# Kernel optimization log

Hardware: AMD Instinct MI355X
Metric: run time of the kernel (lower is better)

Reference implementation:

```python
import jax, jax.numpy as jnp
from jax import lax
import numpy as np

B, N, C = 64, 8732, 81  # batch, anchors (SSD300), classes (COCO+bg)
POS_RATE = 0.003        # keep 3*num_pos < N (argsort column index must be in range)


def setup_inputs() -> dict:
    key = jax.random.key(0)
    k1, k2, k3, k4, k5, k6 = jax.random.split(key, 6)
    pred_conf = jax.random.normal(k1, (B, N, C), dtype=jnp.float32)
    pred_loc = jax.random.normal(k2, (B, N, 4), dtype=jnp.float32)
    # one-hot gt_conf; class 0 = background; sparse positives
    is_pos = jax.random.uniform(k3, (B, N)) < POS_RATE
    labels = jnp.where(is_pos, jax.random.randint(k4, (B, N), 1, C), 0)
    gt_conf = jax.nn.one_hot(labels, C, dtype=jnp.float32)
    gt_loc = jax.random.normal(k5, (B, N, 4), dtype=jnp.float32)
    return {"pred_conf": pred_conf, "pred_loc": pred_loc,
            "gt_conf": gt_conf, "gt_loc": gt_loc}


def reference(pred_conf, pred_loc, gt_conf, gt_loc):
    negative_ratio = 3.0
    # softmax cross entropy per anchor: [B, N]
    log_sm = jax.nn.log_softmax(pred_conf, axis=-1)
    conf_loss = -jnp.sum(log_sm * gt_conf, axis=-1)

    # positive mask (gt background prob == 0 => positive); detached in original
    pos_mask = (lax.stop_gradient(gt_conf)[:, :, 0] == 0).astype(jnp.float32)
    num_pos = jnp.sum(pos_mask)
    positive_conf_loss = pos_mask * conf_loss

    # hard-negative mining (faithful to original, including the quirk that the
    # "threshold" is the argsort INDEX value at column num_negative_conf)
    neg_mask = 1.0 - pos_mask
    cl_neg = lax.stop_gradient(conf_loss) * neg_mask  # detached in original
    order = jnp.argsort(cl_neg, axis=-1)              # [B, N] ascending
    num_neg = (negative_ratio * num_pos).astype(jnp.int32)  # scalar, traced
    idx = jnp.broadcast_to(num_neg, (cl_neg.shape[0], 1))
    thr = jnp.take_along_axis(order, idx, axis=1).astype(jnp.float32)  # [B,1]
    neg_mask = neg_mask * (cl_neg > thr).astype(jnp.float32)
    negative_conf_loss = neg_mask * conf_loss

    conf_total = jnp.sum(positive_conf_loss + negative_conf_loss, axis=-1)  # [B]

    # smooth-L1-ish loc loss (faithful, incl. loc_loss_mask == linear mask bug)
    d = pred_loc - gt_loc
    lin = (jnp.abs(lax.stop_gradient(d)) > 1.0).astype(jnp.float32)
    loc = ((jnp.abs(d) - 0.5) * lin + 0.5 * d * d * (1.0 - lin)) * lin
    loc_total = jnp.sum(loc, axis=(-1, -2))  # [B]

    return conf_total, loc_total
```

## Files before the change

kernel.cpp:

```cpp
#include <hip/hip_runtime.h>
#include <math.h>

#define NCLS 81
#define NANCH 8732
#define NB 64
#define BUCKET_STRIDE 16
#define HSTRIDE 257
#define NCONF_BLK 8732
#define NLOC_BLK  2240

__global__ __launch_bounds__(256) void conf_loc_kernel(
    const float* __restrict__ pred_conf,
    const float* __restrict__ gt_conf,
    const float* __restrict__ pred_loc,
    const float* __restrict__ gt_loc,
    float* __restrict__ cl_out,
    int* __restrict__ pos_buckets,
    float* __restrict__ row_pos,
    float* __restrict__ out)
{
    const int tid = threadIdx.x;
    const int lane = tid & 63, wid = tid >> 6;

    if (blockIdx.x >= NCONF_BLK) {
        const int bid = blockIdx.x - NCONF_BLK;
        const int b = bid & 63;
        const int chunk = bid >> 6;
        const int idx = chunk * 256 + tid;
        float local = 0.f;
        if (idx < NANCH) {
            const float4* p = (const float4*)(pred_loc + (size_t)b * (NANCH * 4));
            const float4* g = (const float4*)(gt_loc + (size_t)b * (NANCH * 4));
            float4 pv = p[idx];
            float4 gv = g[idx];
            float a0 = fabsf(pv.x - gv.x), a1 = fabsf(pv.y - gv.y);
            float a2 = fabsf(pv.z - gv.z), a3 = fabsf(pv.w - gv.w);
            local  = (a0 > 1.f) ? (a0 - 0.5f) : 0.f;
            local += (a1 > 1.f) ? (a1 - 0.5f) : 0.f;
            local += (a2 > 1.f) ? (a2 - 0.5f) : 0.f;
            local += (a3 > 1.f) ? (a3 - 0.5f) : 0.f;
        }
        for (int off = 32; off; off >>= 1) local += __shfl_xor(local, off);
        if (lane == 0 && local != 0.f) atomicAdd(&out[64 + b], local);
        return;
    }

    const int a_loc = tid >> 2;
    const int q = tid & 3;
    const int anchor = blockIdx.x * 64 + a_loc;
    const int h = (4 - (anchor & 3)) & 3;
    const size_t fbase = (size_t)anchor * NCLS;
    const float* xr = pred_conf + fbase;
    const float* gr = gt_conf + fbase;
    const float4* x4 = (const float4*)(xr + h);
    const float4* g4 = (const float4*)(gr + h);
    const int n4 = (NCLS - h) >> 2;

    float se = 0.f, dot = 0.f, g0v = 1.0f;
#pragma unroll
    for (int j = 0; j < 5; ++j) {
        const int k = 4 * j + q;
        if (k < n4) {
            float4 x = x4[k];
            float4 g = g4[k];
            se  += __expf(x.x) + __expf(x.y) + __expf(x.z) + __expf(x.w);
            dot += x.x * g.x + x.y * g.y + x.z * g.z + x.w * g.w;
            if (j == 0 && q == 0 && h == 0) g0v = g.x;
        }
    }
    const int cnt = NCLS - 4 * n4;
    for (int i = q; i < cnt; i += 4) {
        const int e = (i < h) ? i : (h + 4 * n4 + (i - h));
        float xv = xr[e], gv = gr[e];
        se  += __expf(xv);
        dot += xv * gv;
        if (e == 0) g0v = gv;
    }

    se  += __shfl_xor(se, 1);  dot += __shfl_xor(dot, 1);
    se  += __shfl_xor(se, 2);  dot += __shfl_xor(dot, 2);
    const float lse = __logf(se);
    const float conf_loss = lse - dot;

    bool posf = false;
    if (q == 0) {
        posf = (g0v == 0.0f);
        cl_out[anchor] = posf ? 0.0f : conf_loss;
    }

    const int b = anchor / NANCH;
    float contrib = (q == 0 && posf) ? conf_loss : 0.0f;
    int pc = (q == 0 && posf) ? 1 : 0;
    const int bF = __builtin_amdgcn_readfirstlane(b);
    float c0 = (b == bF) ? contrib : 0.0f;
    float c1 = contrib - c0;
    for (int off = 32; off; off >>= 1) {
        c0 += __shfl_xor(c0, off);
        c1 += __shfl_xor(c1, off);
        pc += __shfl_xor(pc, off);
    }
    if (lane == 0) {
        if (c0 != 0.f) atomicAdd(&row_pos[bF], c0);
        if (c1 != 0.f) atomicAdd(&row_pos[bF + 1], c1);
        if (pc) atomicAdd(&pos_buckets[(((blockIdx.x << 2) | wid) & 63) * BUCKET_STRIDE], pc);
    }
}

__global__ __launch_bounds__(1024) void select_kernel(
    const float* __restrict__ val,
    const int* __restrict__ pos_buckets,
    const float* __restrict__ row_pos,
    float* __restrict__ out)
{
    __shared__ float cl[NANCH];
    __shared__ int hist[4 * HSTRIDE];
    __shared__ int wsum[16];
    __shared__ float fred[16];
    __shared__ int sh_numpos;
    __shared__ unsigned int sh_prefix;
    __shared__ int sh_k, sh_thr;

    const int b = blockIdx.x;
    const int tid = threadIdx.x;
    const int lane = tid & 63, w = tid >> 6;
    const int hofs = (w & 3) * HSTRIDE;
    const float* row = val + b * NANCH;

    if (tid < 64) {
        int v = pos_buckets[tid * BUCKET_STRIDE];
        for (int off = 32; off; off >>= 1) v += __shfl_xor(v, off);
        if (tid == 0) sh_numpos = v;
    }
    for (int i = tid; i < NANCH; i += 1024) cl[i] = row[i];
    __syncthreads();

    int k = 3 * sh_numpos;
    if (k > NANCH - 1) k = NANCH - 1;
    if (k < 0) k = 0;

    unsigned int prefix = 0u;
    for (int r = 0; r < 4; ++r) {
        const int shift = 24 - 8 * r;
        const unsigned int maskHigh = (r == 0) ? 0u : (0xFFFFFFFFu << (shift + 8));
        for (int j = tid; j < 4 * HSTRIDE; j += 1024) hist[j] = 0;
        __syncthreads();
        if (r == 0) {
            for (int i0 = 0; i0 < 9216; i0 += 1024) {
                int i = i0 + tid;
                bool valid = (i < NANCH);
                unsigned int u = valid ? __float_as_uint(cl[i]) : 0u;
                int bin = (int)(u >> 24);
                unsigned long long act = __ballot(valid);
                while (act) {
                    int leader = (int)__ffsll((long long)act) - 1;
                    int lbin = __shfl(bin, leader);
                    unsigned long long sm = __ballot(valid && (bin == lbin));
                    if (lane == leader) atomicAdd(&hist[hofs + lbin], (int)__popcll(sm));
                    act &= ~sm;
                }
            }
        } else {
            for (int i = tid; i < NANCH; i += 1024) {
                unsigned int u = __float_as_uint(cl[i]);
                if ((u & maskHigh) == prefix)
                    atomicAdd(&hist[hofs + ((u >> shift) & 0xFF)], 1);
            }
        }
        __syncthreads();
        int h = 0, v = 0;
        if (tid < 256) {
            h = hist[tid] + hist[HSTRIDE + tid] + hist[2 * HSTRIDE + tid]
              + hist[3 * HSTRIDE + tid];
            v = h;
#pragma unroll
            for (int off = 1; off < 64; off <<= 1) {
                int u2 = __shfl_up(v, off);
                if (lane >= off) v += u2;
            }
            if (lane == 63) wsum[w] = v;
        }
        __syncthreads();
        if (tid < 256) {
            int add = 0;
            for (int i = 0; i < w; ++i) add += wsum[i];
            int incl = v + add, excl = incl - h;
            if (excl <= k && k < incl) {
                sh_prefix = prefix | ((unsigned int)tid << shift);
                sh_k = k - excl;
            }
        }
        __syncthreads();
        prefix = sh_prefix;
        k = sh_k;
        __syncthreads();
    }
    const unsigned int T = prefix;

    const int CHUNK = 9;
    int lo = tid * CHUNK; if (lo > NANCH) lo = NANCH;
    int hi = lo + CHUNK; if (hi > NANCH) hi = NANCH;
    int cnt = 0;
    for (int i = lo; i < hi; ++i)
        cnt += (__float_as_uint(cl[i]) == T);
    int v2 = cnt;
#pragma unroll
    for (int off = 1; off < 64; off <<= 1) {
        int u2 = __shfl_up(v2, off);
        if (lane >= off) v2 += u2;
    }
    if (lane == 63) wsum[w] = v2;
    __syncthreads();
    if (tid < 16) {
        int s = wsum[tid];
#pragma unroll
        for (int off = 1; off < 16; off <<= 1) {
            int u2 = __shfl_up(s, off);
            if (lane >= off) s += u2;
        }
        wsum[tid] = s;
    }
    __syncthreads();
    {
        int add = (w == 0) ? 0 : wsum[w - 1];
        int incl = v2 + add, excl = incl - cnt;
        if (excl <= k && k < incl) {
            int need = k - excl, idx = NANCH - 1;
            for (int i = lo; i < hi; ++i) {
                if (__float_as_uint(cl[i]) == T) {
                    if (need == 0) { idx = i; break; }
                    --need;
                }
            }
            sh_thr = idx;
        }
    }
    __syncthreads();

    const float thr = (float)sh_thr;
    float local = 0.f;
    for (int i = tid; i < NANCH; i += 1024) {
        float c = cl[i];
        if (c > thr) local += c;
    }
    for (int off = 32; off; off >>= 1) local += __shfl_xor(local, off);
    if (lane == 0) fred[w] = local;
    __syncthreads();
    if (tid == 0) {
        float t = row_pos[b];
        for (int i = 0; i < 16; ++i) t += fred[i];
        out[b] = t;
    }
}

extern "C" void kernel_launch(void* const* d_in, const int* in_sizes, int n_in,
                              void* d_out, int out_size, void* d_ws, size_t ws_size,
                              hipStream_t stream) {
    const float* pred_conf = (const float*)d_in[0];
    const float* pred_loc  = (const float*)d_in[1];
    const float* gt_conf   = (const float*)d_in[2];
    const float* gt_loc    = (const float*)d_in[3];
    float* out = (float*)d_out;

    int*   pos_buckets = (int*)d_ws;
    float* row_pos     = (float*)((char*)d_ws + 4096);
    float* vals        = (float*)((char*)d_ws + 8192);

    hipMemsetAsync(d_ws, 0, 8192, stream);
    hipMemsetAsync(d_out, 0, 128 * sizeof(float), stream);

    conf_loc_kernel<<<NCONF_BLK + NLOC_BLK, 256, 0, stream>>>(
        pred_conf, gt_conf, pred_loc, gt_loc, vals, pos_buckets, row_pos, out);
    select_kernel<<<NB, 1024, 0, stream>>>(vals, pos_buckets, row_pos, out);
}
```

Measured before the change: 429.8 us.

## Stage pred_conf into LDS via async global loads and exploit one-hot gt labels

Each wave now copies its 16 anchors' logits (1296 floats) straight into shared memory with global_load_lds, replacing the misaligned per-thread float4 loads. While that copy is in flight, gt_conf is scanned for its nonzero entry to get a label per anchor, so the dot product becomes a single indexed lookup. Loss and log-sum-exp are then computed from LDS with three accumulators. This assumes gt_conf is strictly one-hot, since only the last nonzero per anchor is kept, and it adds about 21KB of LDS per block, which may lower occupancy.

```diff
diff --git a/kernel.cpp b/kernel.cpp
--- a/kernel.cpp
+++ b/kernel.cpp
@@ -19,8 +19,11 @@
     float* __restrict__ row_pos,
     float* __restrict__ out)
 {
+    __shared__ float sx[5184];
+    __shared__ int labels[64];
+
     const int tid = threadIdx.x;
-    const int lane = tid & 63, wid = tid >> 6;
+    const int lane = tid & 63, w = tid >> 6;
 
     if (blockIdx.x >= NCONF_BLK) {
         const int bid = blockIdx.x - NCONF_BLK;
@@ -45,64 +48,103 @@
         return;
     }
 
-    const int a_loc = tid >> 2;
-    const int q = tid & 3;
-    const int anchor = blockIdx.x * 64 + a_loc;
-    const int h = (4 - (anchor & 3)) & 3;
-    const size_t fbase = (size_t)anchor * NCLS;
-    const float* xr = pred_conf + fbase;
-    const float* gr = gt_conf + fbase;
-    const float4* x4 = (const float4*)(xr + h);
-    const float4* g4 = (const float4*)(gr + h);
-    const int n4 = (NCLS - h) >> 2;
-
-    float se = 0.f, dot = 0.f, g0v = 1.0f;
-#pragma unroll
-    for (int j = 0; j < 5; ++j) {
-        const int k = 4 * j + q;
-        if (k < n4) {
-            float4 x = x4[k];
-            float4 g = g4[k];
-            se  += __expf(x.x) + __expf(x.y) + __expf(x.z) + __expf(x.w);
-            dot += x.x * g.x + x.y * g.y + x.z * g.z + x.w * g.w;
-            if (j == 0 && q == 0 && h == 0) g0v = g.x;
-        }
-    }
-    const int cnt = NCLS - 4 * n4;
-    for (int i = q; i < cnt; i += 4) {
-        const int e = (i < h) ? i : (h + 4 * n4 + (i - h));
-        float xv = xr[e], gv = gr[e];
-        se  += __expf(xv);
-        dot += xv * gv;
-        if (e == 0) g0v = gv;
-    }
-
-    se  += __shfl_xor(se, 1);  dot += __shfl_xor(dot, 1);
-    se  += __shfl_xor(se, 2);  dot += __shfl_xor(dot, 2);
-    const float lse = __logf(se);
-    const float conf_loss = lse - dot;
-
+    float* sxw = sx + w * 1296;
+    int* labw = labels + w * 16;
+    const size_t gbase = (size_t)blockIdx.x * 5184 + (size_t)w * 1296;
+    const float4* psrc = (const float4*)(pred_conf + gbase);
+    const float4* gsrc = (const float4*)(gt_conf + gbase);
+
+#pragma unroll
+    for (int c = 0; c < 5; ++c) {
+        const int f4 = c * 64 + lane;
+        __builtin_amdgcn_global_load_lds(
+            (const __attribute__((address_space(1))) unsigned int*)(psrc + f4),
+            (__attribute__((address_space(3))) unsigned int*)(&sxw[f4 * 4]),
+            16, 0, 0);
+    }
+    if (lane < 4) {
+        const int f4 = 320 + lane;
+        __builtin_amdgcn_global_load_lds(
+            (const __attribute__((address_space(1))) unsigned int*)(psrc + f4),
+            (__attribute__((address_space(3))) unsigned int*)(&sxw[f4 * 4]),
+            16, 0, 0);
+    }
+
+    int mycnt = 0;
+#pragma unroll
+    for (int c = 0; c < 5; ++c) {
+        const int f4 = c * 64 + lane;
+        float4 g = gsrc[f4];
+        float gv[4] = {g.x, g.y, g.z, g.w};
+#pragma unroll
+        for (int t = 0; t < 4; ++t) {
+            if (gv[t] != 0.0f) {
+                const int e = 4 * f4 + t;
+                const int a = e / 81, cls = e - 81 * a;
+                labw[a] = cls;
+                mycnt += (cls != 0);
+            }
+        }
+    }
+    if (lane < 4) {
+        const int f4 = 320 + lane;
+        float4 g = gsrc[f4];
+        float gv[4] = {g.x, g.y, g.z, g.w};
+#pragma unroll
+        for (int t = 0; t < 4; ++t) {
+            if (gv[t] != 0.0f) {
+                const int e = 4 * f4 + t;
+                const int a = e / 81, cls = e - 81 * a;
+                labw[a] = cls;
+                mycnt += (cls != 0);
+            }
+        }
+    }
+    for (int off = 32; off; off >>= 1) mycnt += __shfl_xor(mycnt, off);
+    if (lane == 0 && mycnt)
+        atomicAdd(&pos_buckets[(((blockIdx.x << 2) | w) & 63) * BUCKET_STRIDE], mycnt);
+
+    asm volatile("s_waitcnt vmcnt(0) lgkmcnt(0)" ::: "memory");
+    __builtin_amdgcn_sched_barrier(0);
+
+    const int a = lane >> 2, q = lane & 3;
+    const float* xr = sxw + a * 81;
+    float s0 = 0.f, s1 = 0.f, s2 = 0.f;
+#pragma unroll
+    for (int j = 0; j < 21; ++j) {
+        const int c = q + 4 * j;
+        if (c < NCLS) {
+            float e = __expf(xr[c]);
+            if (j % 3 == 0) s0 += e; else if (j % 3 == 1) s1 += e; else s2 += e;
+        }
+    }
+    float s = s0 + s1 + s2;
+    s += __shfl_xor(s, 1);
+    s += __shfl_xor(s, 2);
+    const float lse = __logf(s);
+
+    const int anchor = blockIdx.x * 64 + w * 16 + a;
+    float conf_loss = 0.f;
     bool posf = false;
     if (q == 0) {
-        posf = (g0v == 0.0f);
+        const int lbl = labw[a];
+        conf_loss = lse - xr[lbl];
+        posf = (lbl != 0);
         cl_out[anchor] = posf ? 0.0f : conf_loss;
     }
 
     const int b = anchor / NANCH;
-    float contrib = (q == 0 && posf) ? conf_loss : 0.0f;
-    int pc = (q == 0 && posf) ? 1 : 0;
+    const float contrib = posf ? conf_loss : 0.0f;
     const int bF = __builtin_amdgcn_readfirstlane(b);
     float c0 = (b == bF) ? contrib : 0.0f;
     float c1 = contrib - c0;
     for (int off = 32; off; off >>= 1) {
         c0 += __shfl_xor(c0, off);
         c1 += __shfl_xor(c1, off);
-        pc += __shfl_xor(pc, off);
     }
     if (lane == 0) {
         if (c0 != 0.f) atomicAdd(&row_pos[bF], c0);
         if (c1 != 0.f) atomicAdd(&row_pos[bF + 1], c1);
-        if (pc) atomicAdd(&pos_buckets[(((blockIdx.x << 2) | wid) & 63) * BUCKET_STRIDE], pc);
     }
 }
 
```

Result: faster. 420.8 us (-2.1%).

## Persistent double-buffered conf kernel with direct global-to-LDS loads and sparse labels

Applied to the files above, without the earlier changes.

Replaces the one-block-per-64-anchors conf pass with a persistent grid of 1792 blocks. Each block walks 32-anchor tiles, copying pred_conf into a double-buffered LDS tile with global_load_lds while the next tile is prefetched. Instead of a dense dot product with gt_conf, it takes each anchor's label from the nonzero one-hot entry and reads that single logit from LDS. The loc reduction now writes per-block partials that the select kernel sums, removing the loc atomics and the output memset. The hand-placed waitcnt pipelining adds correctness risk, and the label extraction assumes gt_conf is exactly one-hot.

```diff
diff --git a/kernel.cpp b/kernel.cpp
--- a/kernel.cpp
+++ b/kernel.cpp
@@ -6,8 +6,11 @@
 #define NB 64
 #define BUCKET_STRIDE 16
 #define HSTRIDE 257
-#define NCONF_BLK 8732
 #define NLOC_BLK  2240
+#define NCONF_BLK 1792
+#define NTILES 17464
+#define TILE_A 32
+#define WAVE_F 648
 
 __global__ __launch_bounds__(256) void conf_loc_kernel(
     const float* __restrict__ pred_conf,
@@ -17,13 +20,17 @@
     float* __restrict__ cl_out,
     int* __restrict__ pos_buckets,
     float* __restrict__ row_pos,
-    float* __restrict__ out)
+    float* __restrict__ locp)
 {
+    __shared__ float sx[2][2592];
+    __shared__ int labels[2][32];
+    __shared__ float red[4];
+
     const int tid = threadIdx.x;
-    const int lane = tid & 63, wid = tid >> 6;
-
-    if (blockIdx.x >= NCONF_BLK) {
-        const int bid = blockIdx.x - NCONF_BLK;
+    const int lane = tid & 63, w = tid >> 6;
+
+    if (blockIdx.x < NLOC_BLK) {
+        const int bid = blockIdx.x;
         const int b = bid & 63;
         const int chunk = bid >> 6;
         const int idx = chunk * 256 + tid;
@@ -41,75 +48,137 @@
             local += (a3 > 1.f) ? (a3 - 0.5f) : 0.f;
         }
         for (int off = 32; off; off >>= 1) local += __shfl_xor(local, off);
-        if (lane == 0 && local != 0.f) atomicAdd(&out[64 + b], local);
+        if (lane == 0) red[w] = local;
+        __syncthreads();
+        if (tid == 0) locp[bid] = red[0] + red[1] + red[2] + red[3];
         return;
     }
 
-    const int a_loc = tid >> 2;
-    const int q = tid & 3;
-    const int anchor = blockIdx.x * 64 + a_loc;
-    const int h = (4 - (anchor & 3)) & 3;
-    const size_t fbase = (size_t)anchor * NCLS;
-    const float* xr = pred_conf + fbase;
-    const float* gr = gt_conf + fbase;
-    const float4* x4 = (const float4*)(xr + h);
-    const float4* g4 = (const float4*)(gr + h);
-    const int n4 = (NCLS - h) >> 2;
-
-    float se = 0.f, dot = 0.f, g0v = 1.0f;
-#pragma unroll
-    for (int j = 0; j < 5; ++j) {
-        const int k = 4 * j + q;
-        if (k < n4) {
-            float4 x = x4[k];
-            float4 g = g4[k];
-            se  += __expf(x.x) + __expf(x.y) + __expf(x.z) + __expf(x.w);
-            dot += x.x * g.x + x.y * g.y + x.z * g.z + x.w * g.w;
-            if (j == 0 && q == 0 && h == 0) g0v = g.x;
-        }
-    }
-    const int cnt = NCLS - 4 * n4;
-    for (int i = q; i < cnt; i += 4) {
-        const int e = (i < h) ? i : (h + 4 * n4 + (i - h));
-        float xv = xr[e], gv = gr[e];
-        se  += __expf(xv);
-        dot += xv * gv;
-        if (e == 0) g0v = gv;
-    }
-
-    se  += __shfl_xor(se, 1);  dot += __shfl_xor(dot, 1);
-    se  += __shfl_xor(se, 2);  dot += __shfl_xor(dot, 2);
-    const float lse = __logf(se);
-    const float conf_loss = lse - dot;
-
-    bool posf = false;
-    if (q == 0) {
-        posf = (g0v == 0.0f);
-        cl_out[anchor] = posf ? 0.0f : conf_loss;
-    }
-
-    const int b = anchor / NANCH;
-    float contrib = (q == 0 && posf) ? conf_loss : 0.0f;
-    int pc = (q == 0 && posf) ? 1 : 0;
-    const int bF = __builtin_amdgcn_readfirstlane(b);
-    float c0 = (b == bF) ? contrib : 0.0f;
-    float c1 = contrib - c0;
-    for (int off = 32; off; off >>= 1) {
-        c0 += __shfl_xor(c0, off);
-        c1 += __shfl_xor(c1, off);
-        pc += __shfl_xor(pc, off);
-    }
-    if (lane == 0) {
-        if (c0 != 0.f) atomicAdd(&row_pos[bF], c0);
-        if (c1 != 0.f) atomicAdd(&row_pos[bF + 1], c1);
-        if (pc) atomicAdd(&pos_buckets[(((blockIdx.x << 2) | wid) & 63) * BUCKET_STRIDE], pc);
-    }
+    const int pid = blockIdx.x - NLOC_BLK;
+    float* swA = &sx[0][w * WAVE_F];
+    float* swB = &sx[1][w * WAVE_F];
+    int pacc = 0;
+
+#define DMA3(dst, src)                                                              \
+    do {                                                                            \
+        __builtin_amdgcn_global_load_lds(                                           \
+            (const __attribute__((address_space(1))) unsigned int*)((src) + lane),  \
+            (__attribute__((address_space(3))) unsigned int*)(&(dst)[lane * 4]),    \
+            16, 0, 0);                                                              \
+        __builtin_amdgcn_global_load_lds(                                           \
+            (const __attribute__((address_space(1))) unsigned int*)((src) + 64 + lane), \
+            (__attribute__((address_space(3))) unsigned int*)(&(dst)[(64 + lane) * 4]), \
+            16, 0, 0);                                                              \
+        if (lane < 34)                                                              \
+            __builtin_amdgcn_global_load_lds(                                       \
+                (const __attribute__((address_space(1))) unsigned int*)((src) + 128 + lane), \
+                (__attribute__((address_space(3))) unsigned int*)(&(dst)[(128 + lane) * 4]), \
+                16, 0, 0);                                                          \
+    } while (0)
+
+    int T = pid;
+    {
+        const float4* ps = (const float4*)(pred_conf + (size_t)T * 2592 + w * WAVE_F);
+        DMA3(swA, ps);
+    }
+    const float4* gs = (const float4*)(gt_conf + (size_t)T * 2592 + w * WAVE_F);
+    float4 g0 = gs[lane];
+    float4 g1 = gs[64 + lane];
+    float4 g2 = (lane < 34) ? gs[128 + lane] : float4{0.f, 0.f, 0.f, 0.f};
+
+    int cur = 0;
+    for (;;) {
+        const int Tn = T + NCONF_BLK;
+        const bool hasN = (Tn < NTILES);
+        float* swc = cur ? swB : swA;
+        float* swn = cur ? swA : swB;
+
+        if (hasN) {
+            const float4* ps = (const float4*)(pred_conf + (size_t)Tn * 2592 + w * WAVE_F);
+            DMA3(swn, ps);
+            asm volatile("s_waitcnt vmcnt(3)" ::: "memory");
+        } else {
+            asm volatile("s_waitcnt vmcnt(0)" ::: "memory");
+        }
+        __builtin_amdgcn_sched_barrier(0);
+
+        {
+            const float4 gg[3] = {g0, g1, g2};
+#pragma unroll
+            for (int c = 0; c < 3; ++c) {
+                const int f4 = c * 64 + lane;
+                float gv[4] = {gg[c].x, gg[c].y, gg[c].z, gg[c].w};
+#pragma unroll
+                for (int t = 0; t < 4; ++t) {
+                    if (gv[t] != 0.0f) {
+                        const int e = 4 * f4 + t;
+                        const int a = e / 81, cls = e - 81 * a;
+                        labels[cur][w * 8 + a] = cls;
+                        pacc += (cls != 0);
+                    }
+                }
+            }
+        }
+        if (hasN) {
+            const float4* gn = (const float4*)(gt_conf + (size_t)Tn * 2592 + w * WAVE_F);
+            g0 = gn[lane];
+            g1 = gn[64 + lane];
+            g2 = (lane < 34) ? gn[128 + lane] : float4{0.f, 0.f, 0.f, 0.f};
+        }
+        asm volatile("s_waitcnt lgkmcnt(0)" ::: "memory");
+        __builtin_amdgcn_sched_barrier(0);
+
+        {
+            const int a = lane >> 3, r = lane & 7;
+            const float* xr = swc + a * 81;
+            float s = 0.f;
+#pragma unroll
+            for (int j = 0; j < 10; ++j) s += __expf(xr[r + 8 * j]);
+            if (r == 0) s += __expf(xr[80]);
+            s += __shfl_xor(s, 1);
+            s += __shfl_xor(s, 2);
+            s += __shfl_xor(s, 4);
+            const float lse = __logf(s);
+
+            const int anchor = T * TILE_A + w * 8 + a;
+            float contrib = 0.f;
+            if (r == 0) {
+                const int lbl = labels[cur][w * 8 + a];
+                const float cl = lse - xr[lbl];
+                const bool posf = (lbl != 0);
+                cl_out[anchor] = posf ? 0.0f : cl;
+                if (posf) contrib = cl;
+            }
+            const int b = anchor / NANCH;
+            const int bF = __builtin_amdgcn_readfirstlane(b);
+            float c0 = (b == bF) ? contrib : 0.0f;
+            float c1 = contrib - c0;
+            for (int off = 32; off; off >>= 1) {
+                c0 += __shfl_xor(c0, off);
+                c1 += __shfl_xor(c1, off);
+            }
+            if (lane == 0) {
+                if (c0 != 0.f) atomicAdd(&row_pos[bF], c0);
+                if (c1 != 0.f) atomicAdd(&row_pos[bF + 1], c1);
+            }
+        }
+
+        if (!hasN) break;
+        T = Tn;
+        cur ^= 1;
+    }
+#undef DMA3
+
+    for (int off = 32; off; off >>= 1) pacc += __shfl_xor(pacc, off);
+    if (lane == 0 && pacc)
+        atomicAdd(&pos_buckets[(((pid << 2) | w) & 63) * BUCKET_STRIDE], pacc);
 }
 
 __global__ __launch_bounds__(1024) void select_kernel(
     const float* __restrict__ val,
     const int* __restrict__ pos_buckets,
     const float* __restrict__ row_pos,
+    const float* __restrict__ locp,
     float* __restrict__ out)
 {
     __shared__ float cl[NANCH];
@@ -130,6 +199,10 @@
         int v = pos_buckets[tid * BUCKET_STRIDE];
         for (int off = 32; off; off >>= 1) v += __shfl_xor(v, off);
         if (tid == 0) sh_numpos = v;
+    } else if (tid < 128) {
+        float v = (lane < 35) ? locp[lane * 64 + b] : 0.f;
+        for (int off = 32; off; off >>= 1) v += __shfl_xor(v, off);
+        if (lane == 0) out[64 + b] = v;
     }
     for (int i = tid; i < NANCH; i += 1024) cl[i] = row[i];
     __syncthreads();
@@ -263,12 +336,12 @@
 
     int*   pos_buckets = (int*)d_ws;
     float* row_pos     = (float*)((char*)d_ws + 4096);
-    float* vals        = (float*)((char*)d_ws + 8192);
+    float* locp        = (float*)((char*)d_ws + 5120);
+    float* vals        = (float*)((char*)d_ws + 16384);
 
     hipMemsetAsync(d_ws, 0, 8192, stream);
-    hipMemsetAsync(d_out, 0, 128 * sizeof(float), stream);
-
-    conf_loc_kernel<<<NCONF_BLK + NLOC_BLK, 256, 0, stream>>>(
-        pred_conf, gt_conf, pred_loc, gt_loc, vals, pos_buckets, row_pos, out);
-    select_kernel<<<NB, 1024, 0, stream>>>(vals, pos_buckets, row_pos, out);
+
+    conf_loc_kernel<<<NLOC_BLK + NCONF_BLK, 256, 0, stream>>>(
+        pred_conf, gt_conf, pred_loc, gt_loc, vals, pos_buckets, row_pos, locp);
+    select_kernel<<<NB, 1024, 0, stream>>>(vals, pos_buckets, row_pos, locp, out);
 }
```

After: 393.3 us. -8.5%, faster.
